# Kernel optimization log

Measured on AMD Instinct MI355X. Metric: run time of the kernel, lower is better.

Reference implementation:

```python
import jax, jax.numpy as jnp
import numpy as np

B, N, NODE_DIM, COND_DIM, EDGE_DIM = 16, 256, 512, 512, 128
E_TOT = 262144  # total edges, divisible by B
EPS = 1e-5


def weight_norm(v, g):
    # torch weight_norm dim=0: per-output-row normalization. v: [out, in], g: [out]
    return v * (g / jnp.sqrt(jnp.sum(v * v, axis=1)))[:, None]


def setup_inputs() -> dict:
    key = jax.random.key(0)
    ks = jax.random.split(key, 12)
    node_feats = jax.random.normal(ks[0], (B, N, NODE_DIM), dtype=jnp.float32)
    cond_feats = jax.random.normal(ks[1], (B, COND_DIM), dtype=jnp.float32)
    edge_indexes = jnp.sort(jax.random.randint(ks[2], (E_TOT,), 0, B * N * N, dtype=jnp.int64))
    s_node = 1.0 / np.sqrt(NODE_DIM)
    s_cond = 1.0 / np.sqrt(COND_DIM)
    s_film = 1.0 / np.sqrt(2 * EDGE_DIM)
    return {
        "node_feats": node_feats,
        "cond_feats": cond_feats,
        "edge_indexes": edge_indexes,
        "v_node": jax.random.uniform(ks[3], (EDGE_DIM, NODE_DIM), jnp.float32, -s_node, s_node),
        "g_node": jnp.ones((EDGE_DIM,), jnp.float32),
        "b_node": jnp.zeros((EDGE_DIM,), jnp.float32),
        "v_cond": jax.random.uniform(ks[4], (2 * EDGE_DIM, COND_DIM), jnp.float32, -s_cond, s_cond),
        "g_cond": jnp.ones((2 * EDGE_DIM,), jnp.float32),
        "b_cond": jnp.zeros((2 * EDGE_DIM,), jnp.float32),
        "w_film": jax.random.uniform(ks[5], (EDGE_DIM, 2 * EDGE_DIM), jnp.float32, -s_film, s_film),
        "b_film": jnp.zeros((EDGE_DIM,), jnp.float32),
    }


def reference(node_feats, cond_feats, edge_indexes, v_node, g_node, b_node,
              v_cond, g_cond, b_cond, w_film, b_film):
    # node projection: Dropout(0) -> weight_norm Linear -> ReLU
    w_n = weight_norm(v_node, g_node)
    nodes = jax.nn.relu(jnp.einsum('bnd,ed->bne', node_feats, w_n) + b_node)  # [B,N,E]

    # cond projection -> gamma, beta
    w_c = weight_norm(v_cond, g_cond)
    gb = cond_feats @ w_c.T + b_cond  # [B, 2E]
    gamma = gb[:, :EDGE_DIM] + 1.0
    beta = gb[:, EDGE_DIM:]

    # gather edge endpoints directly (equivalent to materializing [B,N,N,2E] 'cat' then indexing)
    b_idx = edge_indexes // (N * N)
    i_idx = (edge_indexes // N) % N
    j_idx = edge_indexes % N
    fused = jnp.concatenate([nodes[b_idx, i_idx], nodes[b_idx, j_idx]], axis=-1)  # [E_TOT, 2E]

    # film_l: linear -> LayerNorm(no affine) -> FiLM -> ReLU, on view (B, E_TOT//B, E)
    x = fused @ w_film.T + b_film  # [E_TOT, EDGE_DIM]
    x = x.reshape(B, E_TOT // B, EDGE_DIM)
    mu = jnp.mean(x, axis=-1, keepdims=True)
    var = jnp.mean(jnp.square(x - mu), axis=-1, keepdims=True)
    x = (x - mu) * jax.lax.rsqrt(var + EPS)
    x = x * gamma[:, None, :] + beta[:, None, :]
    x = jax.nn.relu(x)
    return x.reshape(E_TOT, EDGE_DIM)
```

## Files before the change

### kernel.cpp

```cpp
#include <hip/hip_runtime.h>
#include <hip/hip_bf16.h>

typedef __bf16 bf16_t;
typedef bf16_t bf16x8 __attribute__((ext_vector_type(8)));
typedef bf16_t bf16x4 __attribute__((ext_vector_type(4)));
typedef float f32x4 __attribute__((ext_vector_type(4)));

#define NODE_DIM 512
#define COND_DIM 512
#define EDGE_DIM 128

__global__ __launch_bounds__(256) void cond_scales_kernel(
    const float* __restrict__ cond_feats, const float* __restrict__ v_cond,
    const float* __restrict__ g_cond, const float* __restrict__ b_cond,
    const float* __restrict__ v_node, const float* __restrict__ g_node,
    float* __restrict__ gamma, float* __restrict__ beta,
    float* __restrict__ scale_node)
{
    int lane = threadIdx.x & 63;
    int wv = threadIdx.x >> 6;
    int bid = blockIdx.x;
    if (bid < 1024) {
        int id = bid * 4 + wv;
        int b = id >> 8, n = id & 255;
        const float* cf = cond_feats + b * COND_DIM + lane * 8;
        const float* vc = v_cond + (size_t)n * COND_DIM + lane * 8;
        float dot = 0.f, sq = 0.f;
#pragma unroll
        for (int i = 0; i < 2; i++) {
            float4 c4 = ((const float4*)cf)[i];
            float4 v4 = ((const float4*)vc)[i];
            dot += c4.x * v4.x + c4.y * v4.y + c4.z * v4.z + c4.w * v4.w;
            sq  += v4.x * v4.x + v4.y * v4.y + v4.z * v4.z + v4.w * v4.w;
        }
#pragma unroll
        for (int o = 32; o > 0; o >>= 1) {
            dot += __shfl_xor(dot, o);
            sq  += __shfl_xor(sq, o);
        }
        if (lane == 0) {
            float val = dot * (g_cond[n] * rsqrtf(sq)) + b_cond[n];
            if (n < 128) gamma[b * 128 + n] = val + 1.0f;
            else         beta[b * 128 + (n - 128)] = val;
        }
    } else {
        int id = (bid - 1024) * 4 + wv;
        const float* vn = v_node + (size_t)id * NODE_DIM + lane * 8;
        float sq = 0.f;
#pragma unroll
        for (int i = 0; i < 2; i++) {
            float4 v4 = ((const float4*)vn)[i];
            sq += v4.x * v4.x + v4.y * v4.y + v4.z * v4.z + v4.w * v4.w;
        }
#pragma unroll
        for (int o = 32; o > 0; o >>= 1) sq += __shfl_xor(sq, o);
        if (lane == 0) scale_node[id] = g_node[id] * rsqrtf(sq);
    }
}

__global__ __launch_bounds__(256) void fused_gemm_kernel(
    const float* __restrict__ node_feats, const float* __restrict__ v_node,
    const float* __restrict__ b_node, const float* __restrict__ w_film,
    const float* __restrict__ scale_node, bf16_t* __restrict__ P)
{
    __shared__ __attribute__((aligned(16))) bf16_t A_s[64 * 40];
    __shared__ __attribute__((aligned(16))) bf16_t W_s[256 * 40];
    __shared__ __attribute__((aligned(16))) bf16_t N_s[64 * 136];

    int t = threadIdx.x;
    int lane = t & 63, wv = t >> 6;
    int m0 = blockIdx.x * 64;

    f32x4 zero4 = {0.f, 0.f, 0.f, 0.f};
    f32x4 acc[8];
#pragma unroll
    for (int i = 0; i < 8; i++) acc[i] = zero4;

    const int ar = t >> 2, ak = (t & 3) * 8;
    const int wn = t >> 1, wk = (t & 1) * 16;

    const int arow = wv * 16 + (lane & 15);
    const int kb = (lane >> 4) * 8;
    const int cl = lane & 15;

    for (int ks = 0; ks < 16; ks++) {
        int k0 = ks * 32;
        {
            const float* g = node_feats + (size_t)(m0 + ar) * NODE_DIM + k0 + ak;
            float4 x0 = ((const float4*)g)[0];
            float4 x1 = ((const float4*)g)[1];
            bf16x8 v;
            v[0] = (bf16_t)x0.x; v[1] = (bf16_t)x0.y; v[2] = (bf16_t)x0.z; v[3] = (bf16_t)x0.w;
            v[4] = (bf16_t)x1.x; v[5] = (bf16_t)x1.y; v[6] = (bf16_t)x1.z; v[7] = (bf16_t)x1.w;
            *(bf16x8*)&A_s[ar * 40 + ak] = v;
        }
        {
            const float* g = v_node + (size_t)wn * NODE_DIM + k0 + wk;
#pragma unroll
            for (int h = 0; h < 2; h++) {
                float4 x0 = ((const float4*)g)[2 * h];
                float4 x1 = ((const float4*)g)[2 * h + 1];
                bf16x8 v;
                v[0] = (bf16_t)x0.x; v[1] = (bf16_t)x0.y; v[2] = (bf16_t)x0.z; v[3] = (bf16_t)x0.w;
                v[4] = (bf16_t)x1.x; v[5] = (bf16_t)x1.y; v[6] = (bf16_t)x1.z; v[7] = (bf16_t)x1.w;
                *(bf16x8*)&W_s[wn * 40 + wk + h * 8] = v;
            }
        }
        __syncthreads();
        bf16x8 af = *(const bf16x8*)&A_s[arow * 40 + kb];
#pragma unroll
        for (int nt = 0; nt < 8; nt++) {
            bf16x8 bfr = *(const bf16x8*)&W_s[(nt * 16 + cl) * 40 + kb];
            acc[nt] = __builtin_amdgcn_mfma_f32_16x16x32_bf16(af, bfr, acc[nt], 0, 0, 0);
        }
        __syncthreads();
    }

    {
        int rbase = wv * 16 + ((lane >> 4) << 2);
#pragma unroll
        for (int nt = 0; nt < 8; nt++) {
            int col = nt * 16 + cl;
            float s = scale_node[col], bb = b_node[col];
#pragma unroll
            for (int r = 0; r < 4; r++) {
                float v = fmaxf(acc[nt][r] * s + bb, 0.f);
                N_s[(rbase + r) * 136 + col] = (bf16_t)v;
            }
        }
    }

    f32x4 acc2[16];
#pragma unroll
    for (int i = 0; i < 16; i++) acc2[i] = zero4;

    for (int ks = 0; ks < 4; ks++) {
        int k0 = ks * 32;
        __syncthreads();
        {
            const float* g = (t < 128) ? (w_film + (size_t)t * 256 + k0)
                                       : (w_film + (size_t)(t - 128) * 256 + 128 + k0);
#pragma unroll
            for (int h = 0; h < 4; h++) {
                float4 x0 = ((const float4*)g)[2 * h];
                float4 x1 = ((const float4*)g)[2 * h + 1];
                bf16x8 v;
                v[0] = (bf16_t)x0.x; v[1] = (bf16_t)x0.y; v[2] = (bf16_t)x0.z; v[3] = (bf16_t)x0.w;
                v[4] = (bf16_t)x1.x; v[5] = (bf16_t)x1.y; v[6] = (bf16_t)x1.z; v[7] = (bf16_t)x1.w;
                *(bf16x8*)&W_s[t * 40 + h * 8] = v;
            }
        }
        __syncthreads();
        bf16x8 af = *(const bf16x8*)&N_s[arow * 136 + k0 + kb];
#pragma unroll
        for (int nt = 0; nt < 16; nt++) {
            bf16x8 bfr = *(const bf16x8*)&W_s[(nt * 16 + cl) * 40 + kb];
            acc2[nt] = __builtin_amdgcn_mfma_f32_16x16x32_bf16(af, bfr, acc2[nt], 0, 0, 0);
        }
    }

    {
        int rbase = m0 + wv * 16 + ((lane >> 4) << 2);
#pragma unroll
        for (int nt = 0; nt < 16; nt++) {
            int col = nt * 16 + cl;
#pragma unroll
            for (int r = 0; r < 4; r++) {
                P[(size_t)(rbase + r) * 256 + col] = (bf16_t)acc2[nt][r];
            }
        }
    }
}

__global__ __launch_bounds__(256) void edge_kernel(
    const int* __restrict__ edges, const bf16_t* __restrict__ P,
    const float* __restrict__ gamma, const float* __restrict__ beta,
    const float* __restrict__ b_film, float* __restrict__ out)
{
    int t = threadIdx.x;
    int lane = t & 63, wv = t >> 6;
    int v = (blockIdx.x & 7) * 4096 + (blockIdx.x >> 3);
    int r = v * 8 + wv * 2 + (lane >> 5);
    int hl = lane & 31;
    int c = hl * 4;

    int bb = v >> 11;
    float4 g4  = *(const float4*)&gamma[bb * 128 + c];
    float4 be4 = *(const float4*)&beta[bb * 128 + c];
    float4 bf4 = *(const float4*)&b_film[c];

    int e = edges[r];
    int ri = e >> 8;
    int rj = ((e >> 16) << 8) | (e & 255);

    bf16x4 p1 = *(const bf16x4*)&P[(size_t)ri * 256 + c];
    bf16x4 p2 = *(const bf16x4*)&P[(size_t)rj * 256 + 128 + c];

    float x0 = (float)p1[0] + (float)p2[0] + bf4.x;
    float x1 = (float)p1[1] + (float)p2[1] + bf4.y;
    float x2 = (float)p1[2] + (float)p2[2] + bf4.z;
    float x3 = (float)p1[3] + (float)p2[3] + bf4.w;

    float s  = x0 + x1 + x2 + x3;
    float ss = x0 * x0 + x1 * x1 + x2 * x2 + x3 * x3;
#pragma unroll
    for (int o = 16; o > 0; o >>= 1) {
        s  += __shfl_xor(s, o);
        ss += __shfl_xor(ss, o);
    }
    float mu  = s * (1.0f / 128.0f);
    float var = ss * (1.0f / 128.0f) - mu * mu;
    float rs  = rsqrtf(var + 1e-5f);

    float4 o4;
    o4.x = fmaxf((x0 - mu) * rs * g4.x + be4.x, 0.f);
    o4.y = fmaxf((x1 - mu) * rs * g4.y + be4.y, 0.f);
    o4.z = fmaxf((x2 - mu) * rs * g4.z + be4.z, 0.f);
    o4.w = fmaxf((x3 - mu) * rs * g4.w + be4.w, 0.f);
    *(float4*)&out[(size_t)r * 128 + c] = o4;
}

extern "C" void kernel_launch(void* const* d_in, const int* in_sizes, int n_in,
                              void* d_out, int out_size, void* d_ws, size_t ws_size,
                              hipStream_t stream) {
    const float* node_feats = (const float*)d_in[0];
    const float* cond_feats = (const float*)d_in[1];
    const int*   edges      = (const int*)d_in[2];
    const float* v_node     = (const float*)d_in[3];
    const float* g_node     = (const float*)d_in[4];
    const float* b_node     = (const float*)d_in[5];
    const float* v_cond     = (const float*)d_in[6];
    const float* g_cond     = (const float*)d_in[7];
    const float* b_cond     = (const float*)d_in[8];
    const float* w_film     = (const float*)d_in[9];
    const float* b_film     = (const float*)d_in[10];
    float* out = (float*)d_out;

    char* ws = (char*)d_ws;
    float*  scale_node = (float*)(ws);
    float*  gamma      = (float*)(ws + 4096);
    float*  beta       = (float*)(ws + 4096 + 8192);
    bf16_t* P          = (bf16_t*)(ws + 32768);

    cond_scales_kernel<<<1056, 256, 0, stream>>>(cond_feats, v_cond, g_cond, b_cond,
                                                 v_node, g_node, gamma, beta, scale_node);
    fused_gemm_kernel<<<64, 256, 0, stream>>>(node_feats, v_node, b_node, w_film,
                                              scale_node, P);
    edge_kernel<<<32768, 256, 0, stream>>>(edges, P, gamma, beta, b_film, out);
}
```

Measured before the change: 211.5 us.

## Pre-convert operands to bf16 and split node GEMM into more smaller blocks

Conversion of node_feats, v_node and w_film to bf16 moves into the prep kernel, which writes them to workspace. The node and FiLM GEMM now runs on 256 blocks of 16 rows instead of 64 blocks of 64 rows, reading bf16 operands straight from global memory. Output P is staged through shared memory so it can be written with vectorized stores. This targets the low occupancy of the 64-block GEMM, at the cost of an extra round trip through global memory for the converted inputs.

```diff
diff --git a/kernel.cpp b/kernel.cpp
--- a/kernel.cpp
+++ b/kernel.cpp
@@ -10,18 +10,72 @@
 #define COND_DIM 512
 #define EDGE_DIM 128
 
-__global__ __launch_bounds__(256) void cond_scales_kernel(
-    const float* __restrict__ cond_feats, const float* __restrict__ v_cond,
-    const float* __restrict__ g_cond, const float* __restrict__ b_cond,
+#define WS_A    0x000000
+#define WS_WN   0x400000
+#define WS_WC   0x420000
+#define WS_SC   0x430000
+#define WS_GA   0x431000
+#define WS_BE   0x433000
+#define WS_P    0x440000
+
+__device__ __forceinline__ bf16x8 cvt8(float4 a, float4 b) {
+    bf16x8 v;
+    v[0] = (bf16_t)a.x; v[1] = (bf16_t)a.y; v[2] = (bf16_t)a.z; v[3] = (bf16_t)a.w;
+    v[4] = (bf16_t)b.x; v[5] = (bf16_t)b.y; v[6] = (bf16_t)b.z; v[7] = (bf16_t)b.w;
+    return v;
+}
+
+__global__ __launch_bounds__(256) void prep_kernel(
+    const float* __restrict__ node_feats, const float* __restrict__ cond_feats,
     const float* __restrict__ v_node, const float* __restrict__ g_node,
-    float* __restrict__ gamma, float* __restrict__ beta,
-    float* __restrict__ scale_node)
+    const float* __restrict__ v_cond, const float* __restrict__ g_cond,
+    const float* __restrict__ b_cond, const float* __restrict__ w_film,
+    char* __restrict__ ws)
 {
-    int lane = threadIdx.x & 63;
-    int wv = threadIdx.x >> 6;
+    bf16_t* A  = (bf16_t*)(ws + WS_A);
+    bf16_t* Wn = (bf16_t*)(ws + WS_WN);
+    bf16_t* Wc = (bf16_t*)(ws + WS_WC);
+    float* scale_node = (float*)(ws + WS_SC);
+    float* gamma = (float*)(ws + WS_GA);
+    float* beta  = (float*)(ws + WS_BE);
+
+    int t = threadIdx.x;
     int bid = blockIdx.x;
+    int lane = t & 63, wv = t >> 6;
+
     if (bid < 1024) {
-        int id = bid * 4 + wv;
+        size_t idx = ((size_t)bid * 256 + t) * 8;
+        float4 a = ((const float4*)(node_feats + idx))[0];
+        float4 b = ((const float4*)(node_feats + idx))[1];
+        *(bf16x8*)(A + idx) = cvt8(a, b);
+    } else if (bid < 1056) {
+        size_t idx = ((size_t)(bid - 1024) * 256 + t) * 8;
+        float4 a = ((const float4*)(v_node + idx))[0];
+        float4 b = ((const float4*)(v_node + idx))[1];
+        *(bf16x8*)(Wn + idx) = cvt8(a, b);
+    } else if (bid < 1072) {
+        int u = (bid - 1056) * 256 + t;
+        int n = u >> 4;
+        int ko = (u & 15) * 8;
+        const float* src = (n < 128) ? (w_film + (size_t)n * 256 + ko)
+                                     : (w_film + (size_t)(n - 128) * 256 + 128 + ko);
+        float4 a = ((const float4*)src)[0];
+        float4 b = ((const float4*)src)[1];
+        *(bf16x8*)(Wc + (size_t)n * 128 + ko) = cvt8(a, b);
+    } else if (bid < 1104) {
+        int id = (bid - 1072) * 4 + wv;
+        const float* vn = v_node + (size_t)id * NODE_DIM + lane * 8;
+        float sq = 0.f;
+#pragma unroll
+        for (int i = 0; i < 2; i++) {
+            float4 v4 = ((const float4*)vn)[i];
+            sq += v4.x * v4.x + v4.y * v4.y + v4.z * v4.z + v4.w * v4.w;
+        }
+#pragma unroll
+        for (int o = 32; o > 0; o >>= 1) sq += __shfl_xor(sq, o);
+        if (lane == 0) scale_node[id] = g_node[id] * rsqrtf(sq);
+    } else {
+        int id = (bid - 1104) * 4 + wv;
         int b = id >> 8, n = id & 255;
         const float* cf = cond_feats + b * COND_DIM + lane * 8;
         const float* vc = v_cond + (size_t)n * COND_DIM + lane * 8;
@@ -43,140 +97,102 @@
             if (n < 128) gamma[b * 128 + n] = val + 1.0f;
             else         beta[b * 128 + (n - 128)] = val;
         }
-    } else {
-        int id = (bid - 1024) * 4 + wv;
-        const float* vn = v_node + (size_t)id * NODE_DIM + lane * 8;
-        float sq = 0.f;
-#pragma unroll
-        for (int i = 0; i < 2; i++) {
-            float4 v4 = ((const float4*)vn)[i];
-            sq += v4.x * v4.x + v4.y * v4.y + v4.z * v4.z + v4.w * v4.w;
-        }
-#pragma unroll
-        for (int o = 32; o > 0; o >>= 1) sq += __shfl_xor(sq, o);
-        if (lane == 0) scale_node[id] = g_node[id] * rsqrtf(sq);
-    }
-}
-
-__global__ __launch_bounds__(256) void fused_gemm_kernel(
-    const float* __restrict__ node_feats, const float* __restrict__ v_node,
-    const float* __restrict__ b_node, const float* __restrict__ w_film,
-    const float* __restrict__ scale_node, bf16_t* __restrict__ P)
+    }
+}
+
+__global__ __launch_bounds__(256) void gemm_kernel(
+    const float* __restrict__ b_node, char* __restrict__ ws)
 {
-    __shared__ __attribute__((aligned(16))) bf16_t A_s[64 * 40];
-    __shared__ __attribute__((aligned(16))) bf16_t W_s[256 * 40];
-    __shared__ __attribute__((aligned(16))) bf16_t N_s[64 * 136];
+    const bf16_t* A  = (const bf16_t*)(ws + WS_A);
+    const bf16_t* Wn = (const bf16_t*)(ws + WS_WN);
+    const bf16_t* Wc = (const bf16_t*)(ws + WS_WC);
+    const float* scale_node = (const float*)(ws + WS_SC);
+    bf16_t* P = (bf16_t*)(ws + WS_P);
+
+    __shared__ __attribute__((aligned(16))) bf16_t N_s[16 * 136];
+    __shared__ __attribute__((aligned(16))) float  T_s[4][16][68];
 
     int t = threadIdx.x;
-    int lane = t & 63, wv = t >> 6;
-    int m0 = blockIdx.x * 64;
+    int lane = t & 63, w = t >> 6;
+    int r16 = lane & 15, half = lane >> 4;
+    int m0 = blockIdx.x * 16;
 
     f32x4 zero4 = {0.f, 0.f, 0.f, 0.f};
-    f32x4 acc[8];
-#pragma unroll
-    for (int i = 0; i < 8; i++) acc[i] = zero4;
-
-    const int ar = t >> 2, ak = (t & 3) * 8;
-    const int wn = t >> 1, wk = (t & 1) * 16;
-
-    const int arow = wv * 16 + (lane & 15);
-    const int kb = (lane >> 4) * 8;
-    const int cl = lane & 15;
-
-    for (int ks = 0; ks < 16; ks++) {
-        int k0 = ks * 32;
-        {
-            const float* g = node_feats + (size_t)(m0 + ar) * NODE_DIM + k0 + ak;
-            float4 x0 = ((const float4*)g)[0];
-            float4 x1 = ((const float4*)g)[1];
-            bf16x8 v;
-            v[0] = (bf16_t)x0.x; v[1] = (bf16_t)x0.y; v[2] = (bf16_t)x0.z; v[3] = (bf16_t)x0.w;
-            v[4] = (bf16_t)x1.x; v[5] = (bf16_t)x1.y; v[6] = (bf16_t)x1.z; v[7] = (bf16_t)x1.w;
-            *(bf16x8*)&A_s[ar * 40 + ak] = v;
-        }
-        {
-            const float* g = v_node + (size_t)wn * NODE_DIM + k0 + wk;
-#pragma unroll
-            for (int h = 0; h < 2; h++) {
-                float4 x0 = ((const float4*)g)[2 * h];
-                float4 x1 = ((const float4*)g)[2 * h + 1];
-                bf16x8 v;
-                v[0] = (bf16_t)x0.x; v[1] = (bf16_t)x0.y; v[2] = (bf16_t)x0.z; v[3] = (bf16_t)x0.w;
-                v[4] = (bf16_t)x1.x; v[5] = (bf16_t)x1.y; v[6] = (bf16_t)x1.z; v[7] = (bf16_t)x1.w;
-                *(bf16x8*)&W_s[wn * 40 + wk + h * 8] = v;
-            }
-        }
-        __syncthreads();
-        bf16x8 af = *(const bf16x8*)&A_s[arow * 40 + kb];
-#pragma unroll
-        for (int nt = 0; nt < 8; nt++) {
-            bf16x8 bfr = *(const bf16x8*)&W_s[(nt * 16 + cl) * 40 + kb];
-            acc[nt] = __builtin_amdgcn_mfma_f32_16x16x32_bf16(af, bfr, acc[nt], 0, 0, 0);
-        }
-        __syncthreads();
-    }
-
-    {
-        int rbase = wv * 16 + ((lane >> 4) << 2);
-#pragma unroll
-        for (int nt = 0; nt < 8; nt++) {
-            int col = nt * 16 + cl;
+
+    f32x4 acc0 = zero4, acc1 = zero4;
+    {
+        const bf16_t* aptr = A + (size_t)(m0 + r16) * NODE_DIM + half * 8;
+        const bf16_t* bptr = Wn + (size_t)(w * 32 + r16) * NODE_DIM + half * 8;
+#pragma unroll
+        for (int ks = 0; ks < 16; ks++) {
+            bf16x8 af = *(const bf16x8*)(aptr + ks * 32);
+            bf16x8 b0 = *(const bf16x8*)(bptr + ks * 32);
+            bf16x8 b1 = *(const bf16x8*)(bptr + 16 * NODE_DIM + ks * 32);
+            acc0 = __builtin_amdgcn_mfma_f32_16x16x32_bf16(af, b0, acc0, 0, 0, 0);
+            acc1 = __builtin_amdgcn_mfma_f32_16x16x32_bf16(af, b1, acc1, 0, 0, 0);
+        }
+    }
+    {
+        int rbase = half * 4;
+#pragma unroll
+        for (int j = 0; j < 2; j++) {
+            int col = w * 32 + j * 16 + r16;
             float s = scale_node[col], bb = b_node[col];
+            f32x4 a = j ? acc1 : acc0;
 #pragma unroll
             for (int r = 0; r < 4; r++) {
-                float v = fmaxf(acc[nt][r] * s + bb, 0.f);
+                float v = fmaxf(a[r] * s + bb, 0.f);
                 N_s[(rbase + r) * 136 + col] = (bf16_t)v;
             }
         }
     }
-
-    f32x4 acc2[16];
-#pragma unroll
-    for (int i = 0; i < 16; i++) acc2[i] = zero4;
-
-    for (int ks = 0; ks < 4; ks++) {
-        int k0 = ks * 32;
-        __syncthreads();
-        {
-            const float* g = (t < 128) ? (w_film + (size_t)t * 256 + k0)
-                                       : (w_film + (size_t)(t - 128) * 256 + 128 + k0);
-#pragma unroll
-            for (int h = 0; h < 4; h++) {
-                float4 x0 = ((const float4*)g)[2 * h];
-                float4 x1 = ((const float4*)g)[2 * h + 1];
-                bf16x8 v;
-                v[0] = (bf16_t)x0.x; v[1] = (bf16_t)x0.y; v[2] = (bf16_t)x0.z; v[3] = (bf16_t)x0.w;
-                v[4] = (bf16_t)x1.x; v[5] = (bf16_t)x1.y; v[6] = (bf16_t)x1.z; v[7] = (bf16_t)x1.w;
-                *(bf16x8*)&W_s[t * 40 + h * 8] = v;
+    __syncthreads();
+
+    f32x4 acc2[4];
+#pragma unroll
+    for (int i = 0; i < 4; i++) acc2[i] = zero4;
+    {
+        const bf16_t* bptr = Wc + (size_t)(w * 64 + r16) * 128 + half * 8;
+#pragma unroll
+        for (int ks = 0; ks < 4; ks++) {
+            bf16x8 af = *(const bf16x8*)&N_s[r16 * 136 + ks * 32 + half * 8];
+#pragma unroll
+            for (int j = 0; j < 4; j++) {
+                bf16x8 bf = *(const bf16x8*)(bptr + j * 16 * 128 + ks * 32);
+                acc2[j] = __builtin_amdgcn_mfma_f32_16x16x32_bf16(af, bf, acc2[j], 0, 0, 0);
             }
         }
-        __syncthreads();
-        bf16x8 af = *(const bf16x8*)&N_s[arow * 136 + k0 + kb];
-#pragma unroll
-        for (int nt = 0; nt < 16; nt++) {
-            bf16x8 bfr = *(const bf16x8*)&W_s[(nt * 16 + cl) * 40 + kb];
-            acc2[nt] = __builtin_amdgcn_mfma_f32_16x16x32_bf16(af, bfr, acc2[nt], 0, 0, 0);
-        }
-    }
-
-    {
-        int rbase = m0 + wv * 16 + ((lane >> 4) << 2);
-#pragma unroll
-        for (int nt = 0; nt < 16; nt++) {
-            int col = nt * 16 + cl;
-#pragma unroll
-            for (int r = 0; r < 4; r++) {
-                P[(size_t)(rbase + r) * 256 + col] = (bf16_t)acc2[nt][r];
-            }
+    }
+    {
+        int rbase = half * 4;
+#pragma unroll
+        for (int j = 0; j < 4; j++) {
+            int col = j * 16 + r16;
+#pragma unroll
+            for (int r = 0; r < 4; r++) T_s[w][rbase + r][col] = acc2[j][r];
+        }
+    }
+    __syncthreads();
+    {
+#pragma unroll
+        for (int r2 = 0; r2 < 2; r2++) {
+            int row = r2 * 8 + (lane >> 3);
+            int colg = (lane & 7) * 8;
+            float4 a = *(const float4*)&T_s[w][row][colg];
+            float4 b = *(const float4*)&T_s[w][row][colg + 4];
+            *(bf16x8*)&P[(size_t)(m0 + row) * 256 + w * 64 + colg] = cvt8(a, b);
         }
     }
 }
 
 __global__ __launch_bounds__(256) void edge_kernel(
-    const int* __restrict__ edges, const bf16_t* __restrict__ P,
-    const float* __restrict__ gamma, const float* __restrict__ beta,
+    const int* __restrict__ edges, const char* __restrict__ ws,
     const float* __restrict__ b_film, float* __restrict__ out)
 {
+    const bf16_t* P = (const bf16_t*)(ws + WS_P);
+    const float* gamma = (const float*)(ws + WS_GA);
+    const float* beta  = (const float*)(ws + WS_BE);
+
     int t = threadIdx.x;
     int lane = t & 63, wv = t >> 6;
     int v = (blockIdx.x & 7) * 4096 + (blockIdx.x >> 3);
@@ -235,16 +251,10 @@
     const float* w_film     = (const float*)d_in[9];
     const float* b_film     = (const float*)d_in[10];
     float* out = (float*)d_out;
-
     char* ws = (char*)d_ws;
-    float*  scale_node = (float*)(ws);
-    float*  gamma      = (float*)(ws + 4096);
-    float*  beta       = (float*)(ws + 4096 + 8192);
-    bf16_t* P          = (bf16_t*)(ws + 32768);
-
-    cond_scales_kernel<<<1056, 256, 0, stream>>>(cond_feats, v_cond, g_cond, b_cond,
-                                                 v_node, g_node, gamma, beta, scale_node);
-    fused_gemm_kernel<<<64, 256, 0, stream>>>(node_feats, v_node, b_node, w_film,
-                                              scale_node, P);
-    edge_kernel<<<32768, 256, 0, stream>>>(edges, P, gamma, beta, b_film, out);
-}
+
+    prep_kernel<<<2128, 256, 0, stream>>>(node_feats, cond_feats, v_node, g_node,
+                                          v_cond, g_cond, b_cond, w_film, ws);
+    gemm_kernel<<<256, 256, 0, stream>>>(b_node, ws);
+    edge_kernel<<<32768, 256, 0, stream>>>(edges, ws, b_film, out);
+}
```

After: 195.2 us, median of 2. -7.7%, faster.
